# Optimization experiments

Hardware: AMD Instinct MI355X
Metric: run time of the kernel (lower is better)

The kernel has to match this reference:

```python
import jax, jax.numpy as jnp
import numpy as np

B, S, D, H, O, E, K = 8, 2048, 768, 3072, 768, 8, 2
LN_EPS = 1e-5


def setup_inputs() -> dict:
    key = jax.random.key(0)
    ks = jax.random.split(key, 8)
    x = jax.random.normal(ks[0], (B, S, D), dtype=jnp.float32)
    router_w = jax.random.normal(ks[1], (D, E), dtype=jnp.float32) * 0.02
    router_b = jnp.zeros((E,), dtype=jnp.float32)
    w1 = jax.random.normal(ks[2], (E, D, H), dtype=jnp.float32) * 0.02
    b1 = jnp.zeros((E, H), dtype=jnp.float32)
    w2 = jax.random.normal(ks[3], (E, H, O), dtype=jnp.float32) * 0.02
    b2 = jnp.zeros((E, O), dtype=jnp.float32)
    ln_g = jnp.ones((O,), dtype=jnp.float32)
    ln_b = jnp.zeros((O,), dtype=jnp.float32)
    return {"x": x, "router_w": router_w, "router_b": router_b,
            "w1": w1, "b1": b1, "w2": w2, "b2": b2,
            "ln_g": ln_g, "ln_b": ln_b}


def _layernorm(y, g, b):
    mu = jnp.mean(y, axis=-1, keepdims=True)
    var = jnp.mean(jnp.square(y - mu), axis=-1, keepdims=True)
    return (y - mu) * jax.lax.rsqrt(var + LN_EPS) * g + b


def reference(x, router_w, router_b, w1, b1, w2, b2, ln_g, ln_b):
    # Router (NoisyTopKRouter, eval mode: no noise): top-k gate over expert logits
    logits = jnp.einsum('bsd,de->bse', x, router_w) + router_b   # [B,S,E]
    top_vals, top_idx = jax.lax.top_k(logits, K)                 # [B,S,K]
    routing_weights = jax.nn.softmax(top_vals, axis=-1)          # [B,S,K]

    out = jnp.zeros((B, S, O), dtype=x.dtype)
    for e in range(E):
        # per-token combined weight for this expert (0 if not routed)
        w_e = jnp.sum(routing_weights * (top_idx == e), axis=-1)  # [B,S]
        # dense per-expert feedforward on ALL tokens (as in original loop)
        h = jax.nn.gelu(jnp.einsum('bsd,dh->bsh', x, w1[e]) + b1[e])
        y = jnp.einsum('bsh,ho->bso', h, w2[e]) + b2[e]
        out = out + y * w_e[..., None]
    return _layernorm(out, ln_g, ln_b)
```

## Files before the change

kernel.cpp:

```cpp
#include <hip/hip_runtime.h>
#include <hip/hip_bf16.h>
#include <stdint.h>

#define Bq  8
#define Sq  2048
#define Dq  768
#define Hq  3072
#define Oq  768
#define Eq  8
#define Mq  (Bq*Sq)
#define LN_EPS 1e-5f
#define MAX_TILES (2*Mq/128 + 16)

typedef unsigned short u16;
typedef __attribute__((ext_vector_type(4))) float f32x4;
typedef __attribute__((ext_vector_type(8))) __bf16 bf16x8;

static __device__ __forceinline__ u16 f2bf(float f) {
  __hip_bfloat16 h = __float2bfloat16(f);
  return __builtin_bit_cast(u16, h);
}

static __device__ __forceinline__ float gelu_f(float x) {
  float u = 0.7978845608028654f * x * (1.0f + 0.044715f * x * x);
  float e = __expf(2.0f * u);
  float t = 1.0f - 2.0f / (e + 1.0f);
  return 0.5f * x * (1.0f + t);
}

typedef const __attribute__((address_space(1))) void* gas_t;
typedef __attribute__((address_space(3))) void* las_t;
static __device__ __forceinline__ void gload16(const void* g, void* l) {
  __builtin_amdgcn_global_load_lds((gas_t)g, (las_t)l, 16, 0, 0);
}

__global__ __launch_bounds__(256) void router_cvt_kernel(
    const float* __restrict__ x, const float* __restrict__ rw,
    const float* __restrict__ rb, u16* __restrict__ Xbf,
    int* __restrict__ tok_seg, float2* __restrict__ tok_w)
{
  __shared__ float rwT[Eq * Dq];
  for (int i = threadIdx.x; i < Eq * Dq; i += 256)
    rwT[(i & 7) * Dq + (i >> 3)] = rw[i];
  __syncthreads();

  int wid = threadIdx.x >> 6;
  int lane = threadIdx.x & 63;
  int token = blockIdx.x * 4 + wid;
  const float4* xrow = (const float4*)(x + (size_t)token * Dq);
  ushort4* orow = (ushort4*)(Xbf + (size_t)token * Dq);

  float acc[Eq];
#pragma unroll
  for (int e = 0; e < Eq; e++) acc[e] = 0.f;

#pragma unroll
  for (int it = 0; it < Dq / 256; it++) {
    int d4 = it * 64 + lane;
    float4 xv = xrow[d4];
    ushort4 o;
    o.x = f2bf(xv.x); o.y = f2bf(xv.y); o.z = f2bf(xv.z); o.w = f2bf(xv.w);
    orow[d4] = o;
    int d = d4 * 4;
#pragma unroll
    for (int e = 0; e < Eq; e++) {
      float4 wv = *(const float4*)&rwT[e * Dq + d];
      acc[e] += xv.x * wv.x + xv.y * wv.y + xv.z * wv.z + xv.w * wv.w;
    }
  }
#pragma unroll
  for (int e = 0; e < Eq; e++) {
    float v = acc[e];
#pragma unroll
    for (int off = 32; off; off >>= 1) v += __shfl_xor(v, off);
    acc[e] = v;
  }
  if (lane == 0) {
    float v1 = -1e30f, v2 = -1e30f; int i1 = 0, i2 = 0;
#pragma unroll
    for (int e = 0; e < Eq; e++) {
      float v = acc[e] + rb[e];
      if (v > v1)      { v2 = v1; i2 = i1; v1 = v; i1 = e; }
      else if (v > v2) { v2 = v;  i2 = e; }
    }
    float ex = expf(v2 - v1);
    float wa = 1.f / (1.f + ex);
    float wb = ex / (1.f + ex);
    tok_seg[token] = i1 | ((8 + i2) << 8);
    tok_w[token] = make_float2(wa, wb);
  }
}

__global__ __launch_bounds__(256) void scatter_build(
    const int* __restrict__ tok_seg, const float2* __restrict__ tok_w,
    int* __restrict__ cnt, int* __restrict__ seg_tok, float* __restrict__ seg_wgt)
{
  __shared__ int histA[16], histB[16], base[16];
  int t = threadIdx.x;
  if (t < 16) { histA[t] = 0; histB[t] = 0; }
  __syncthreads();
  int token = blockIdx.x * 256 + t;
  int sp = tok_seg[token];
  float2 wv = tok_w[token];
  int s0 = sp & 0xff, s1 = sp >> 8;
  atomicAdd(&histA[s0], 1);
  atomicAdd(&histA[s1], 1);
  __syncthreads();
  if (t < 16) base[t] = atomicAdd(&cnt[t], histA[t]);
  __syncthreads();
  int p0 = base[s0] + atomicAdd(&histB[s0], 1);
  seg_tok[(size_t)s0 * Mq + p0] = token;
  seg_wgt[(size_t)s0 * Mq + p0] = wv.x;
  int p1 = base[s1] + atomicAdd(&histB[s1], 1);
  seg_tok[(size_t)s1 * Mq + p1] = token;
  seg_wgt[(size_t)s1 * Mq + p1] = wv.y;
}

__global__ void prefix_kernel(const int* __restrict__ cnt, int* __restrict__ prefix)
{
  if (threadIdx.x == 0 && blockIdx.x == 0) {
    int t = 0;
#pragma unroll
    for (int s = 0; s < 16; s++) { prefix[s] = t; t += (cnt[s] + 127) >> 7; }
    prefix[16] = t;
  }
}

__global__ __launch_bounds__(256) void transpose_cvt(
    const float* __restrict__ in, u16* __restrict__ out, int R, int C)
{
  __shared__ float tile[32][33];
  int e = blockIdx.z;
  in  += (size_t)e * R * C;
  out += (size_t)e * R * C;
  int c0 = blockIdx.x * 32, r0 = blockIdx.y * 32;
  int tx = threadIdx.x & 31, ty = threadIdx.x >> 5;
#pragma unroll
  for (int rr = 0; rr < 32; rr += 8)
    tile[rr + ty][tx] = in[(size_t)(r0 + rr + ty) * C + c0 + tx];
  __syncthreads();
#pragma unroll
  for (int rr = 0; rr < 32; rr += 8)
    out[(size_t)(c0 + rr + ty) * R + r0 + tx] = f2bf(tile[tx][rr + ty]);
}

template<int EPI>
__global__ __launch_bounds__(256) void moe_gemm(
    const u16* __restrict__ A, const u16* __restrict__ W,
    const float* __restrict__ bias,
    u16* __restrict__ Hout, float* __restrict__ out,
    const int* __restrict__ cnt, const int* __restrict__ prefix,
    const int* __restrict__ seg_tok, const float* __restrict__ seg_wgt,
    int K, int N, int tile_lo)
{
  const int NP = N / 128;
  const int lid = (int)blockIdx.x + NP * (int)blockIdx.y;
  const int xcd = lid & 7, slot = lid >> 3;
  const int t_loc = xcd + 8 * (slot / NP);
  const int panel = slot % NP;

  const int t = tile_lo + t_loc;
  const int total = prefix[16];
  if (t >= total) return;
  int seg = 0;
#pragma unroll
  for (int s = 1; s < 16; s++) if (prefix[s] <= t) seg = s;
  const int e = seg & 7;
  const int segcnt = cnt[seg];
  const int ti = t - prefix[seg];
  const int lt = t_loc;

  __shared__ u16 As[2][128 * 32];
  __shared__ u16 Bs[2][128 * 32];
  const int tid  = threadIdx.x;
  const int lane = tid & 63;
  const int wid  = tid >> 6;
  const int wr   = wid >> 1, wc = wid & 1;
  const int lrow = lane & 15, kgrp = lane >> 4;
  const int kx   = kgrp ^ ((lrow >> 1) & 3);
  const int n0 = panel * 128;

  f32x4 acc[4][4];
#pragma unroll
  for (int m = 0; m < 4; m++)
#pragma unroll
    for (int n = 0; n < 4; n++) acc[m][n] = (f32x4){0.f, 0.f, 0.f, 0.f};

  const int r0 = tid >> 2;
  const int kc = (((tid & 3) ^ ((tid >> 3) & 3)) * 8);
  const u16 *gA0, *gA1;
  if (EPI == 0) {
    int i0 = ti * 128 + r0, i1 = i0 + 64;
    int tok0 = (i0 < segcnt) ? seg_tok[(size_t)seg * Mq + i0] : 0;
    int tok1 = (i1 < segcnt) ? seg_tok[(size_t)seg * Mq + i1] : 0;
    gA0 = A + (size_t)tok0 * K + kc;
    gA1 = A + (size_t)tok1 * K + kc;
  } else {
    gA0 = A + (size_t)(lt * 128 + r0) * K + kc;
    gA1 = gA0 + (size_t)64 * K;
  }
  const u16* gB = W + (size_t)e * K * N + (size_t)(n0 + r0) * K + kc;
  const size_t rowskipB = (size_t)64 * K;
  const int lofs = tid * 8;

  auto stage = [&](int b) {
    gload16(gA0, &As[b][lofs]);
    gload16(gA1, &As[b][lofs + 2048]);
    gload16(gB,            &Bs[b][lofs]);
    gload16(gB + rowskipB, &Bs[b][lofs + 2048]);
    gA0 += 32; gA1 += 32; gB += 32;
  };

  const int NIT = K / 32;
  stage(0);
  for (int it = 0; it < NIT; ++it) {
    const int cur = it & 1;
    if (it + 1 < NIT) {
      stage(cur ^ 1);
      asm volatile("s_waitcnt vmcnt(4)" ::: "memory");
    } else {
      asm volatile("s_waitcnt vmcnt(0)" ::: "memory");
    }
    __builtin_amdgcn_s_barrier();
    __builtin_amdgcn_sched_barrier(0);
    bf16x8 a[4], b[4];
#pragma unroll
    for (int m = 0; m < 4; m++)
      a[m] = *(const bf16x8*)&As[cur][(wr * 64 + m * 16 + lrow) * 32 + kx * 8];
#pragma unroll
    for (int n = 0; n < 4; n++)
      b[n] = *(const bf16x8*)&Bs[cur][(wc * 64 + n * 16 + lrow) * 32 + kx * 8];
#pragma unroll
    for (int m = 0; m < 4; m++)
#pragma unroll
      for (int n = 0; n < 4; n++)
        acc[m][n] = __builtin_amdgcn_mfma_f32_16x16x32_bf16(a[m], b[n], acc[m][n], 0, 0, 0);
    __builtin_amdgcn_sched_barrier(0);
    __builtin_amdgcn_s_barrier();
  }

  const int rbase = wr * 64;
  const int cbase = n0 + wc * 64;
  if (EPI == 0) {
#pragma unroll
    for (int n = 0; n < 4; n++) {
      int c = cbase + n * 16 + lrow;
      float bv = bias[(size_t)e * N + c];
#pragma unroll
      for (int m = 0; m < 4; m++)
#pragma unroll
        for (int j = 0; j < 4; j++) {
          int r = rbase + m * 16 + kgrp * 4 + j;
          float v = acc[m][n][j] + bv;
          Hout[(size_t)(lt * 128 + r) * N + c] = f2bf(gelu_f(v));
        }
    }
  } else {
#pragma unroll
    for (int m = 0; m < 4; m++)
#pragma unroll
      for (int j = 0; j < 4; j++) {
        int r = rbase + m * 16 + kgrp * 4 + j;
        int i = ti * 128 + r;
        if (i < segcnt) {
          int token = seg_tok[(size_t)seg * Mq + i];
          float w = seg_wgt[(size_t)seg * Mq + i];
          float* orow = out + (size_t)token * Oq;
#pragma unroll
          for (int n = 0; n < 4; n++) {
            int c = cbase + n * 16 + lrow;
            float v = (acc[m][n][j] + bias[(size_t)e * N + c]) * w;
            unsafeAtomicAdd(&orow[c], v);
          }
        }
      }
  }
}

__global__ __launch_bounds__(256) void ln_kernel(
    float* __restrict__ io, const float* __restrict__ g, const float* __restrict__ b)
{
  int wid = threadIdx.x >> 6, lane = threadIdx.x & 63;
  int row = blockIdx.x * 4 + wid;
  float* p = io + (size_t)row * Oq;
  float v[Oq / 64];
  float s = 0.f;
#pragma unroll
  for (int i = 0; i < Oq / 64; i++) { v[i] = p[lane + i * 64]; s += v[i]; }
#pragma unroll
  for (int off = 32; off; off >>= 1) s += __shfl_xor(s, off);
  float mu = s * (1.0f / Oq);
  float q = 0.f;
#pragma unroll
  for (int i = 0; i < Oq / 64; i++) { float d = v[i] - mu; q += d * d; }
#pragma unroll
  for (int off = 32; off; off >>= 1) q += __shfl_xor(q, off);
  float inv = rsqrtf(q * (1.0f / Oq) + LN_EPS);
#pragma unroll
  for (int i = 0; i < Oq / 64; i++) {
    int c = lane + i * 64;
    p[c] = (v[i] - mu) * inv * g[c] + b[c];
  }
}

extern "C" void kernel_launch(void* const* d_in, const int* in_sizes, int n_in,
                              void* d_out, int out_size, void* d_ws, size_t ws_size,
                              hipStream_t stream)
{
  const float* x    = (const float*)d_in[0];
  const float* rw   = (const float*)d_in[1];
  const float* rb   = (const float*)d_in[2];
  const float* w1   = (const float*)d_in[3];
  const float* b1   = (const float*)d_in[4];
  const float* w2   = (const float*)d_in[5];
  const float* b2   = (const float*)d_in[6];
  const float* ln_g = (const float*)d_in[7];
  const float* ln_b = (const float*)d_in[8];
  float* out = (float*)d_out;

  char* ws = (char*)d_ws;
  size_t off = 0;
  auto alloc = [&](size_t bytes) {
    void* p = ws + off;
    off += (bytes + 255) & ~(size_t)255;
    return p;
  };
  int*    cnt     = (int*)alloc(16 * 4);
  int*    prefix  = (int*)alloc(17 * 4);
  int*    tok_seg = (int*)alloc((size_t)Mq * 4);
  float2* tok_w   = (float2*)alloc((size_t)Mq * 8);
  int*    seg_tok = (int*)alloc((size_t)16 * Mq * 4);
  float*  seg_wgt = (float*)alloc((size_t)16 * Mq * 4);
  u16* Xbf = (u16*)alloc((size_t)Mq * Dq * 2);
  u16* W1T = (u16*)alloc((size_t)Eq * Dq * Hq * 2);
  u16* W2T = (u16*)alloc((size_t)Eq * Hq * Oq * 2);

  size_t remain = (ws_size > off) ? ws_size - off : 0;
  size_t tile_bytes = (size_t)128 * Hq * 2;
  long long wt = (long long)(remain / tile_bytes);
  if (wt > MAX_TILES) wt = MAX_TILES;
  wt &= ~7LL;
  if (wt < 8) wt = 8;
  int WT = (int)wt;
  u16* Hbuf = (u16*)alloc((size_t)WT * tile_bytes);

  hipMemsetAsync(out, 0, (size_t)Mq * Oq * 4, stream);
  hipMemsetAsync(cnt, 0, 16 * 4, stream);
  router_cvt_kernel<<<Mq / 4, 256, 0, stream>>>(x, rw, rb, Xbf, tok_seg, tok_w);
  scatter_build<<<Mq / 256, 256, 0, stream>>>(tok_seg, tok_w, cnt, seg_tok, seg_wgt);
  prefix_kernel<<<1, 64, 0, stream>>>(cnt, prefix);
  transpose_cvt<<<dim3(Hq / 32, Dq / 32, Eq), 256, 0, stream>>>(w1, W1T, Dq, Hq);
  transpose_cvt<<<dim3(Oq / 32, Hq / 32, Eq), 256, 0, stream>>>(w2, W2T, Hq, Oq);

  for (int tl = 0; tl < MAX_TILES; tl += WT) {
    int gx = MAX_TILES - tl; if (gx > WT) gx = WT;
    moe_gemm<0><<<dim3(Hq / 128, gx), 256, 0, stream>>>(
        Xbf, W1T, b1, Hbuf, nullptr, cnt, prefix, seg_tok, seg_wgt,
        Dq, Hq, tl);
    moe_gemm<1><<<dim3(Oq / 128, gx), 256, 0, stream>>>(
        Hbuf, W2T, b2, nullptr, out, cnt, prefix, seg_tok, seg_wgt,
        Hq, Oq, tl);
  }
  ln_kernel<<<Mq / 4, 256, 0, stream>>>(out, ln_g, ln_b);
}
```

Measured before the change: 740.1 us.

## Use 256x256 tiles with 8-wave phased pipeline for first expert GEMM

The first expert GEMM moves from a 128x128 tile with 4 waves to a 256x256 tile with 8 waves and a K-step of 64. Loads are split into four phases interleaved with MFMA groups, with priority raising and an XOR swizzle on shared memory. Segment tiles are now 256 tokens, and the second GEMM maps two 128-row subtiles onto each 256-row tile. This is meant to raise arithmetic intensity and overlap loads with compute. In exchange it uses more shared memory and registers, and pads more rows in small segments.

```diff
diff --git a/kernel.cpp b/kernel.cpp
--- a/kernel.cpp
+++ b/kernel.cpp
@@ -10,7 +10,7 @@
 #define Eq  8
 #define Mq  (Bq*Sq)
 #define LN_EPS 1e-5f
-#define MAX_TILES (2*Mq/128 + 16)
+#define MAX_T256 (Mq/128 + 16)
 
 typedef unsigned short u16;
 typedef __attribute__((ext_vector_type(4))) float f32x4;
@@ -121,7 +121,7 @@
   if (threadIdx.x == 0 && blockIdx.x == 0) {
     int t = 0;
 #pragma unroll
-    for (int s = 0; s < 16; s++) { prefix[s] = t; t += (cnt[s] + 127) >> 7; }
+    for (int s = 0; s < 16; s++) { prefix[s] = t; t += (cnt[s] + 255) >> 8; }
     prefix[16] = t;
   }
 }
@@ -144,24 +144,20 @@
     out[(size_t)(c0 + rr + ty) * R + r0 + tx] = f2bf(tile[tx][rr + ty]);
 }
 
-template<int EPI>
-__global__ __launch_bounds__(256) void moe_gemm(
+__global__ __launch_bounds__(512, 2) void moe_gemm1(
     const u16* __restrict__ A, const u16* __restrict__ W,
-    const float* __restrict__ bias,
-    u16* __restrict__ Hout, float* __restrict__ out,
+    const float* __restrict__ bias, u16* __restrict__ Hout,
     const int* __restrict__ cnt, const int* __restrict__ prefix,
-    const int* __restrict__ seg_tok, const float* __restrict__ seg_wgt,
-    int K, int N, int tile_lo)
-{
-  const int NP = N / 128;
+    const int* __restrict__ seg_tok, int K, int N, int tile_lo)
+{
+  const int NP = N / 256;
   const int lid = (int)blockIdx.x + NP * (int)blockIdx.y;
   const int xcd = lid & 7, slot = lid >> 3;
   const int t_loc = xcd + 8 * (slot / NP);
   const int panel = slot % NP;
 
   const int t = tile_lo + t_loc;
-  const int total = prefix[16];
-  if (t >= total) return;
+  if (t >= prefix[16]) return;
   int seg = 0;
 #pragma unroll
   for (int s = 1; s < 16; s++) if (prefix[s] <= t) seg = s;
@@ -169,6 +165,158 @@
   const int segcnt = cnt[seg];
   const int ti = t - prefix[seg];
   const int lt = t_loc;
+
+  __shared__ u16 As[2][16384];
+  __shared__ u16 Bs[2][16384];
+  const int tid  = threadIdx.x;
+  const int lane = tid & 63;
+  const int wid  = tid >> 6;
+  const int wr   = wid >> 2, wc = wid & 3;
+  const int lrow = lane & 15, kgrp = lane >> 4;
+  const int gcx0 = ((kgrp)     ^ (lrow & 7)) * 8;
+  const int gcx1 = ((4 + kgrp) ^ (lrow & 7)) * 8;
+
+  f32x4 acc[8][4];
+#pragma unroll
+  for (int m = 0; m < 8; m++)
+#pragma unroll
+    for (int n = 0; n < 4; n++) acc[m][n] = (f32x4){0.f, 0.f, 0.f, 0.f};
+
+  const int srow = tid >> 3;
+  const int swz  = ((tid & 7) ^ (srow & 7)) * 8;
+  const u16 *pA00, *pA01, *pA10, *pA11, *pB00, *pB01, *pB10, *pB11;
+  {
+    int sr;
+    sr = ti * 256 +   0 +  0 + srow;
+    pA00 = A + (size_t)((sr < segcnt) ? seg_tok[(size_t)seg * Mq + sr] : 0) * K + swz;
+    sr = ti * 256 +   0 + 64 + srow;
+    pA01 = A + (size_t)((sr < segcnt) ? seg_tok[(size_t)seg * Mq + sr] : 0) * K + swz;
+    sr = ti * 256 + 128 +  0 + srow;
+    pA10 = A + (size_t)((sr < segcnt) ? seg_tok[(size_t)seg * Mq + sr] : 0) * K + swz;
+    sr = ti * 256 + 128 + 64 + srow;
+    pA11 = A + (size_t)((sr < segcnt) ? seg_tok[(size_t)seg * Mq + sr] : 0) * K + swz;
+    const u16* Wb = W + (size_t)e * K * N;
+    pB00 = Wb + (size_t)(panel * 256 +   0 +  0 + srow) * K + swz;
+    pB01 = Wb + (size_t)(panel * 256 +   0 + 64 + srow) * K + swz;
+    pB10 = Wb + (size_t)(panel * 256 + 128 +  0 + srow) * K + swz;
+    pB11 = Wb + (size_t)(panel * 256 + 128 + 64 + srow) * K + swz;
+  }
+
+#define STG(buf, h, P0, P1)                                \
+  do {                                                     \
+    gload16(P0, &(buf)[(h) * 8192 + tid * 8]);             \
+    gload16(P1, &(buf)[(h) * 8192 + 4096 + tid * 8]);      \
+    P0 += 64; P1 += 64;                                    \
+  } while (0)
+
+  const int NKT = K / 64;
+  STG(As[0], 0, pA00, pA01); STG(As[0], 1, pA10, pA11);
+  STG(Bs[0], 0, pB00, pB01); STG(Bs[0], 1, pB10, pB11);
+
+  bf16x8 bfr[4][2];
+  for (int kt = 0; kt < NKT; ++kt) {
+    const int s = kt & 1, d = s ^ 1;
+    const bool more = (kt + 1 < NKT);
+    const int abase = wr * 128 + lrow;
+    const int bbase = wc * 64 + lrow;
+
+    if (more) {
+      STG(As[d], 0, pA00, pA01);
+      asm volatile("s_waitcnt vmcnt(2)" ::: "memory");
+    } else {
+      asm volatile("s_waitcnt vmcnt(0)" ::: "memory");
+    }
+    __builtin_amdgcn_s_barrier();
+    __builtin_amdgcn_sched_barrier(0);
+#pragma unroll
+    for (int n = 0; n < 4; n++) {
+      bfr[n][0] = *(const bf16x8*)&Bs[s][(bbase + n * 16) * 64 + gcx0];
+      bfr[n][1] = *(const bf16x8*)&Bs[s][(bbase + n * 16) * 64 + gcx1];
+    }
+    {
+      bf16x8 a00 = *(const bf16x8*)&As[s][(abase +  0) * 64 + gcx0];
+      bf16x8 a01 = *(const bf16x8*)&As[s][(abase +  0) * 64 + gcx1];
+      bf16x8 a10 = *(const bf16x8*)&As[s][(abase + 16) * 64 + gcx0];
+      bf16x8 a11 = *(const bf16x8*)&As[s][(abase + 16) * 64 + gcx1];
+      __builtin_amdgcn_s_setprio(1);
+#pragma unroll
+      for (int n = 0; n < 4; n++) {
+        acc[0][n] = __builtin_amdgcn_mfma_f32_16x16x32_bf16(a00, bfr[n][0], acc[0][n], 0, 0, 0);
+        acc[0][n] = __builtin_amdgcn_mfma_f32_16x16x32_bf16(a01, bfr[n][1], acc[0][n], 0, 0, 0);
+        acc[1][n] = __builtin_amdgcn_mfma_f32_16x16x32_bf16(a10, bfr[n][0], acc[1][n], 0, 0, 0);
+        acc[1][n] = __builtin_amdgcn_mfma_f32_16x16x32_bf16(a11, bfr[n][1], acc[1][n], 0, 0, 0);
+      }
+      __builtin_amdgcn_s_setprio(0);
+    }
+    __builtin_amdgcn_sched_barrier(0);
+    __builtin_amdgcn_s_barrier();
+
+#define PHASE(q, STGSTMT)                                                     \
+    do {                                                                      \
+      bf16x8 a00 = *(const bf16x8*)&As[s][(abase + (2*(q))    * 16) * 64 + gcx0]; \
+      bf16x8 a01 = *(const bf16x8*)&As[s][(abase + (2*(q))    * 16) * 64 + gcx1]; \
+      bf16x8 a10 = *(const bf16x8*)&As[s][(abase + (2*(q)+1)  * 16) * 64 + gcx0]; \
+      bf16x8 a11 = *(const bf16x8*)&As[s][(abase + (2*(q)+1)  * 16) * 64 + gcx1]; \
+      if (more) { STGSTMT; }                                                  \
+      __builtin_amdgcn_s_setprio(1);                                          \
+      _Pragma("unroll")                                                       \
+      for (int n = 0; n < 4; n++) {                                           \
+        acc[2*(q)][n]   = __builtin_amdgcn_mfma_f32_16x16x32_bf16(a00, bfr[n][0], acc[2*(q)][n], 0, 0, 0);   \
+        acc[2*(q)][n]   = __builtin_amdgcn_mfma_f32_16x16x32_bf16(a01, bfr[n][1], acc[2*(q)][n], 0, 0, 0);   \
+        acc[2*(q)+1][n] = __builtin_amdgcn_mfma_f32_16x16x32_bf16(a10, bfr[n][0], acc[2*(q)+1][n], 0, 0, 0); \
+        acc[2*(q)+1][n] = __builtin_amdgcn_mfma_f32_16x16x32_bf16(a11, bfr[n][1], acc[2*(q)+1][n], 0, 0, 0); \
+      }                                                                       \
+      __builtin_amdgcn_s_setprio(0);                                          \
+      __builtin_amdgcn_sched_barrier(0);                                      \
+      __builtin_amdgcn_s_barrier();                                           \
+    } while (0)
+
+    PHASE(1, STG(As[d], 1, pA10, pA11));
+    PHASE(2, STG(Bs[d], 0, pB00, pB01));
+    PHASE(3, STG(Bs[d], 1, pB10, pB11));
+#undef PHASE
+  }
+
+  const int rbase = wr * 128;
+  const int cbase = panel * 256 + wc * 64;
+#pragma unroll
+  for (int n = 0; n < 4; n++) {
+    int c = cbase + n * 16 + lrow;
+    float bv = bias[(size_t)e * N + c];
+#pragma unroll
+    for (int m = 0; m < 8; m++)
+#pragma unroll
+      for (int j = 0; j < 4; j++) {
+        int r = rbase + m * 16 + kgrp * 4 + j;
+        float v = acc[m][n][j] + bv;
+        Hout[(size_t)(lt * 256 + r) * N + c] = f2bf(gelu_f(v));
+      }
+  }
+#undef STG
+}
+
+__global__ __launch_bounds__(256) void moe_gemm2(
+    const u16* __restrict__ A, const u16* __restrict__ W,
+    const float* __restrict__ bias, float* __restrict__ out,
+    const int* __restrict__ cnt, const int* __restrict__ prefix,
+    const int* __restrict__ seg_tok, const float* __restrict__ seg_wgt,
+    int K, int N, int tile_lo)
+{
+  const int NP = N / 128;
+  const int lid = (int)blockIdx.x + NP * (int)blockIdx.y;
+  const int xcd = lid & 7, slot = lid >> 3;
+  const int t2 = xcd + 8 * (slot / NP);
+  const int panel = slot % NP;
+
+  const int t256 = tile_lo + (t2 >> 1);
+  if (t256 >= prefix[16]) return;
+  int seg = 0;
+#pragma unroll
+  for (int s = 1; s < 16; s++) if (prefix[s] <= t256) seg = s;
+  const int e = seg & 7;
+  const int segcnt = cnt[seg];
+  const int ti = (t256 - prefix[seg]) * 2 + (t2 & 1);
+  const int lt = t2;
 
   __shared__ u16 As[2][128 * 32];
   __shared__ u16 Bs[2][128 * 32];
@@ -188,17 +336,8 @@
 
   const int r0 = tid >> 2;
   const int kc = (((tid & 3) ^ ((tid >> 3) & 3)) * 8);
-  const u16 *gA0, *gA1;
-  if (EPI == 0) {
-    int i0 = ti * 128 + r0, i1 = i0 + 64;
-    int tok0 = (i0 < segcnt) ? seg_tok[(size_t)seg * Mq + i0] : 0;
-    int tok1 = (i1 < segcnt) ? seg_tok[(size_t)seg * Mq + i1] : 0;
-    gA0 = A + (size_t)tok0 * K + kc;
-    gA1 = A + (size_t)tok1 * K + kc;
-  } else {
-    gA0 = A + (size_t)(lt * 128 + r0) * K + kc;
-    gA1 = gA0 + (size_t)64 * K;
-  }
+  const u16* gA0 = A + (size_t)(lt * 128 + r0) * K + kc;
+  const u16* gA1 = gA0 + (size_t)64 * K;
   const u16* gB = W + (size_t)e * K * N + (size_t)(n0 + r0) * K + kc;
   const size_t rowskipB = (size_t)64 * K;
   const int lofs = tid * 8;
@@ -241,40 +380,24 @@
 
   const int rbase = wr * 64;
   const int cbase = n0 + wc * 64;
-  if (EPI == 0) {
-#pragma unroll
-    for (int n = 0; n < 4; n++) {
-      int c = cbase + n * 16 + lrow;
-      float bv = bias[(size_t)e * N + c];
-#pragma unroll
-      for (int m = 0; m < 4; m++)
-#pragma unroll
-        for (int j = 0; j < 4; j++) {
-          int r = rbase + m * 16 + kgrp * 4 + j;
-          float v = acc[m][n][j] + bv;
-          Hout[(size_t)(lt * 128 + r) * N + c] = f2bf(gelu_f(v));
-        }
-    }
-  } else {
-#pragma unroll
-    for (int m = 0; m < 4; m++)
-#pragma unroll
-      for (int j = 0; j < 4; j++) {
-        int r = rbase + m * 16 + kgrp * 4 + j;
-        int i = ti * 128 + r;
-        if (i < segcnt) {
-          int token = seg_tok[(size_t)seg * Mq + i];
-          float w = seg_wgt[(size_t)seg * Mq + i];
-          float* orow = out + (size_t)token * Oq;
-#pragma unroll
-          for (int n = 0; n < 4; n++) {
-            int c = cbase + n * 16 + lrow;
-            float v = (acc[m][n][j] + bias[(size_t)e * N + c]) * w;
-            unsafeAtomicAdd(&orow[c], v);
-          }
+#pragma unroll
+  for (int m = 0; m < 4; m++)
+#pragma unroll
+    for (int j = 0; j < 4; j++) {
+      int r = rbase + m * 16 + kgrp * 4 + j;
+      int i = ti * 128 + r;
+      if (i < segcnt) {
+        int token = seg_tok[(size_t)seg * Mq + i];
+        float w = seg_wgt[(size_t)seg * Mq + i];
+        float* orow = out + (size_t)token * Oq;
+#pragma unroll
+        for (int n = 0; n < 4; n++) {
+          int c = cbase + n * 16 + lrow;
+          float v = (acc[m][n][j] + bias[(size_t)e * N + c]) * w;
+          unsafeAtomicAdd(&orow[c], v);
         }
       }
-  }
+    }
 }
 
 __global__ __launch_bounds__(256) void ln_kernel(
@@ -336,9 +459,9 @@
   u16* W2T = (u16*)alloc((size_t)Eq * Hq * Oq * 2);
 
   size_t remain = (ws_size > off) ? ws_size - off : 0;
-  size_t tile_bytes = (size_t)128 * Hq * 2;
+  size_t tile_bytes = (size_t)256 * Hq * 2;
   long long wt = (long long)(remain / tile_bytes);
-  if (wt > MAX_TILES) wt = MAX_TILES;
+  if (wt > MAX_T256) wt = MAX_T256;
   wt &= ~7LL;
   if (wt < 8) wt = 8;
   int WT = (int)wt;
@@ -352,14 +475,12 @@
   transpose_cvt<<<dim3(Hq / 32, Dq / 32, Eq), 256, 0, stream>>>(w1, W1T, Dq, Hq);
   transpose_cvt<<<dim3(Oq / 32, Hq / 32, Eq), 256, 0, stream>>>(w2, W2T, Hq, Oq);
 
-  for (int tl = 0; tl < MAX_TILES; tl += WT) {
-    int gx = MAX_TILES - tl; if (gx > WT) gx = WT;
-    moe_gemm<0><<<dim3(Hq / 128, gx), 256, 0, stream>>>(
-        Xbf, W1T, b1, Hbuf, nullptr, cnt, prefix, seg_tok, seg_wgt,
-        Dq, Hq, tl);
-    moe_gemm<1><<<dim3(Oq / 128, gx), 256, 0, stream>>>(
-        Hbuf, W2T, b2, nullptr, out, cnt, prefix, seg_tok, seg_wgt,
-        Hq, Oq, tl);
+  for (int tl = 0; tl < MAX_T256; tl += WT) {
+    int gx = MAX_T256 - tl; if (gx > WT) gx = WT;
+    moe_gemm1<<<dim3(Hq / 256, gx), 512, 0, stream>>>(
+        Xbf, W1T, b1, Hbuf, cnt, prefix, seg_tok, Dq, Hq, tl);
+    moe_gemm2<<<dim3(Oq / 128, 2 * gx), 256, 0, stream>>>(
+        Hbuf, W2T, b2, out, cnt, prefix, seg_tok, seg_wgt, Hq, Oq, tl);
   }
   ln_kernel<<<Mq / 4, 256, 0, stream>>>(out, ln_g, ln_b);
 }
```

Measured after the change: 755.1 us. +2.0%, slower.
